# Performance work log

Hardware: AMD Instinct MI355X
Metric: run time of the kernel (lower is better)

## Reference

```python
import jax, jax.numpy as jnp
import numpy as np

HEADS = 12
DIM_HEAD = 64
WINDOW = 16
SHIFT = 1  # fixed stand-in for random.randint(0, window-1)
SCALE = DIM_HEAD ** -0.5


def window_cls_mask(n, window, shift):
    # Shifted block-diagonal mask over the n-1 non-CLS tokens, CLS attends/attended everywhere.
    size = n - 1
    idx = jnp.arange(size)
    cur = (idx - shift) % window
    left = jnp.clip(idx - cur, 0, size)
    right = jnp.clip(idx + (window - cur), 0, size)
    i = idx[:, None]  # query position
    wmask = (i >= left[None, :]) & (i < right[None, :])  # [size, size]
    full = jnp.ones((n, n), dtype=bool)
    full = full.at[1:, 1:].set(wmask)
    return full  # [n, n] bool


def setup_inputs() -> dict:
    key = jax.random.key(0)
    k1, k2, k3 = jax.random.split(key, 3)
    b, n, dim = 2, 2049, 768
    inner = HEADS * DIM_HEAD
    return {
        "x": jax.random.normal(k1, (b, n, dim), dtype=jnp.float32),
        "w_qkv": jax.random.normal(k2, (dim, 3 * inner), dtype=jnp.float32) * 0.02,
        "w_out": jax.random.normal(k3, (inner, dim), dtype=jnp.float32) * 0.02,
        "b_out": jnp.zeros((dim,), dtype=jnp.float32),
    }


def reference(x, w_qkv, w_out, b_out):
    b, n, dim = x.shape
    h, d = HEADS, DIM_HEAD
    qkv = x @ w_qkv  # [b, n, 3*h*d]
    q, k, v = jnp.split(qkv, 3, axis=-1)
    # b n (h d) -> b h n d
    reshape = lambda t: t.reshape(b, n, h, d).transpose(0, 2, 1, 3)
    q, k, v = reshape(q), reshape(k), reshape(v)
    dots = jnp.einsum('bhid,bhjd->bhij', q, k) * SCALE  # [b, h, n, n]
    mask = window_cls_mask(n, WINDOW, SHIFT)  # [n, n]
    neg = -jnp.finfo(dots.dtype).max
    dots = jnp.where(mask[None, None], dots, neg)
    attn = jax.nn.softmax(dots, axis=-1)
    out = jnp.einsum('bhij,bhjd->bhid', attn, v)  # [b, h, n, d]
    out = out.transpose(0, 2, 1, 3).reshape(b, n, h * d)
    return out @ w_out + b_out
```

## Files before the change

kernel.cpp:

```cpp
#include <hip/hip_runtime.h>
#include <hip/hip_bf16.h>
#include <math.h>

typedef __attribute__((ext_vector_type(8))) __bf16 bf16x8;
typedef __attribute__((ext_vector_type(4))) float f32x4;

#define HEADS 12
#define DHEAD 64
#define NTOK 2049
#define BATCH 2
#define DIM 768
#define QKV3 2304
#define MROWS 4098
#define MP 4224
#define ATT_SCALE 0.125f
#define BKS 64
#define NSPLIT 33
#define PSTRIDE 68

#define CVT_BLOCKS 1584
#define TQKV_BX 72
#define TQKV_BLOCKS (72 * 24)
#define TOUT_BX 24
#define TOUT_BLOCKS (24 * 24)
#define PREP_BLOCKS (CVT_BLOCKS + TQKV_BLOCKS + TOUT_BLOCKS)
#define WIN_BLOCKS (BATCH * 129 * 3)

__global__ __launch_bounds__(256) void prep_kernel(const float* __restrict__ x,
                                                   const float* __restrict__ w_qkv,
                                                   const float* __restrict__ w_out,
                                                   __bf16* __restrict__ xb,
                                                   __bf16* __restrict__ wqkvT,
                                                   __bf16* __restrict__ woutT) {
  __shared__ float tile[32][33];
  const int b = blockIdx.x, tid = threadIdx.x;
  if (b < CVT_BLOCKS) {
    long e = ((long)b * 256 + tid) * 8;
    int row = (int)(e / DIM);
    bf16x8 v;
    if (row < MROWS) {
      const float4 a = *(const float4*)(x + e);
      const float4 c = *(const float4*)(x + e + 4);
      v[0] = (__bf16)a.x; v[1] = (__bf16)a.y; v[2] = (__bf16)a.z; v[3] = (__bf16)a.w;
      v[4] = (__bf16)c.x; v[5] = (__bf16)c.y; v[6] = (__bf16)c.z; v[7] = (__bf16)c.w;
    } else {
#pragma unroll
      for (int j = 0; j < 8; ++j) v[j] = (__bf16)0.f;
    }
    *(bf16x8*)(xb + e) = v;
    return;
  }
  const float* in;
  __bf16* outp;
  int C, bx, by;
  if (b < CVT_BLOCKS + TQKV_BLOCKS) {
    int idx = b - CVT_BLOCKS;
    bx = idx % TQKV_BX; by = idx / TQKV_BX;
    in = w_qkv; outp = wqkvT; C = QKV3;
  } else {
    int idx = b - CVT_BLOCKS - TQKV_BLOCKS;
    bx = idx % TOUT_BX; by = idx / TOUT_BX;
    in = w_out; outp = woutT; C = DIM;
  }
  const int R = DIM;
  const int c0 = bx * 32, r0 = by * 32;
  const int tx = tid & 31, ty = tid >> 5;
#pragma unroll
  for (int i = 0; i < 4; ++i) {
    int r = ty + i * 8;
    tile[r][tx] = in[(size_t)(r0 + r) * C + c0 + tx];
  }
  __syncthreads();
#pragma unroll
  for (int i = 0; i < 4; ++i) {
    int r = ty + i * 8;
    outp[(size_t)(c0 + r) * R + r0 + tx] = (__bf16)tile[tx][r];
  }
}

__global__ __launch_bounds__(256) void gemm_qkv_kernel(const __bf16* __restrict__ A,
                                                       const __bf16* __restrict__ Bt,
                                                       __bf16* __restrict__ C) {
  __shared__ __bf16 sA[2][64 * BKS];
  __shared__ __bf16 sB[2][128 * BKS];
  const int tid = threadIdx.x;
  const int w = tid >> 6, lane = tid & 63;
  const int m0 = blockIdx.y * 64, n0 = blockIdx.x * 128;
  const int wr = w >> 1, wc = w & 1;
  const int K = DIM;
  f32x4 acc[2][4] = {};

  const int srow = (w << 3) + (lane >> 3);
  const int scolE = ((lane & 7) ^ (lane >> 3)) << 3;
  const __bf16* gA = A + (size_t)(m0 + srow) * K + scolE;
  const __bf16* gB = Bt + (size_t)(n0 + srow) * K + scolE;
  const int nk = K / BKS;

#define STAGE_Q(buf, kt)                                                                 \
  do {                                                                                   \
    _Pragma("unroll")                                                                    \
    for (int it = 0; it < 2; ++it) {                                                     \
      __builtin_amdgcn_global_load_lds(                                                  \
          (const __attribute__((address_space(1))) void*)(gA + (size_t)(it * 32) * K + (kt)), \
          (__attribute__((address_space(3))) void*)(&sA[buf][(it << 11) + (w << 9)]), 16, 0, 0); \
    }                                                                                    \
    _Pragma("unroll")                                                                    \
    for (int it = 0; it < 4; ++it) {                                                     \
      __builtin_amdgcn_global_load_lds(                                                  \
          (const __attribute__((address_space(1))) void*)(gB + (size_t)(it * 32) * K + (kt)), \
          (__attribute__((address_space(3))) void*)(&sB[buf][(it << 11) + (w << 9)]), 16, 0, 0); \
    }                                                                                    \
  } while (0)

  STAGE_Q(0, 0);
  __syncthreads();

  const int sw0 = ((lane >> 4) ^ (lane & 7)) << 3;
  const int sw1 = sw0 ^ 32;
  const int rofA = (wr * 32 + (lane & 15)) * BKS;
  const int rofB = (wc * 64 + (lane & 15)) * BKS;

  for (int t = 0; t < nk; ++t) {
    const int cur = t & 1;
    if (t + 1 < nk) STAGE_Q(cur ^ 1, (t + 1) * BKS);
    const __bf16* bufA = sA[cur];
    const __bf16* bufB = sB[cur];
#pragma unroll
    for (int kk = 0; kk < BKS; kk += 32) {
      const int so = (kk == 0) ? sw0 : sw1;
      bf16x8 af[2], bfr[4];
#pragma unroll
      for (int m = 0; m < 2; ++m)
        af[m] = *(const bf16x8*)&bufA[rofA + m * 16 * BKS + so];
#pragma unroll
      for (int n = 0; n < 4; ++n)
        bfr[n] = *(const bf16x8*)&bufB[rofB + n * 16 * BKS + so];
#pragma unroll
      for (int m = 0; m < 2; ++m)
#pragma unroll
        for (int n = 0; n < 4; ++n)
          acc[m][n] = __builtin_amdgcn_mfma_f32_16x16x32_bf16(af[m], bfr[n], acc[m][n], 0, 0, 0);
    }
    __syncthreads();
  }
#undef STAGE_Q

#pragma unroll
  for (int m = 0; m < 2; ++m) {
#pragma unroll
    for (int n = 0; n < 4; ++n) {
      int col = n0 + wc * 64 + n * 16 + (lane & 15);
      int rbase = m0 + wr * 32 + m * 16 + ((lane >> 4) << 2);
#pragma unroll
      for (int r = 0; r < 4; ++r) {
        C[(size_t)(rbase + r) * QKV3 + col] = (__bf16)acc[m][n][r];
      }
    }
  }
}

__global__ __launch_bounds__(256) void gemm_out_kernel(const __bf16* __restrict__ A,
                                                       const __bf16* __restrict__ Bt,
                                                       float* __restrict__ Cv,
                                                       const float* __restrict__ bias) {
  __shared__ __bf16 sA[2][64 * BKS];
  __shared__ __bf16 sB[2][64 * BKS];
  const int tid = threadIdx.x;
  const int w = tid >> 6, lane = tid & 63;
  const int m0 = blockIdx.y * 64, n0 = blockIdx.x * 64;
  const int wr = w >> 1, wc = w & 1;
  const int K = DIM, N = DIM;
  f32x4 acc[2][2] = {};

  const int srow = (w << 3) + (lane >> 3);
  const int scol = ((lane & 7) ^ (lane >> 3)) << 3;
  const __bf16* gA = A + (size_t)(m0 + srow) * K + scol;
  const __bf16* gB = Bt + (size_t)(n0 + srow) * K + scol;
  const int nk = K / BKS;

#define STAGE_O(buf, kt)                                                                 \
  do {                                                                                   \
    _Pragma("unroll")                                                                    \
    for (int it = 0; it < 2; ++it) {                                                     \
      __builtin_amdgcn_global_load_lds(                                                  \
          (const __attribute__((address_space(1))) void*)(gA + (size_t)(it * 32) * K + (kt)), \
          (__attribute__((address_space(3))) void*)(&sA[buf][(it << 11) + (w << 9)]), 16, 0, 0); \
      __builtin_amdgcn_global_load_lds(                                                  \
          (const __attribute__((address_space(1))) void*)(gB + (size_t)(it * 32) * K + (kt)), \
          (__attribute__((address_space(3))) void*)(&sB[buf][(it << 11) + (w << 9)]), 16, 0, 0); \
    }                                                                                    \
  } while (0)

  STAGE_O(0, 0);
  __syncthreads();

  const int sw0 = ((lane >> 4) ^ (lane & 7)) << 3;
  const int sw1 = sw0 ^ 32;
  const int rofA = (wr * 32 + (lane & 15)) * BKS;
  const int rofB = (wc * 32 + (lane & 15)) * BKS;

  for (int t = 0; t < nk; ++t) {
    const int cur = t & 1;
    if (t + 1 < nk) STAGE_O(cur ^ 1, (t + 1) * BKS);
    const __bf16* bufA = sA[cur];
    const __bf16* bufB = sB[cur];
#pragma unroll
    for (int kk = 0; kk < BKS; kk += 32) {
      const int so = (kk == 0) ? sw0 : sw1;
      bf16x8 af[2], bfr[2];
#pragma unroll
      for (int m = 0; m < 2; ++m)
        af[m] = *(const bf16x8*)&bufA[rofA + m * 16 * BKS + so];
#pragma unroll
      for (int n = 0; n < 2; ++n)
        bfr[n] = *(const bf16x8*)&bufB[rofB + n * 16 * BKS + so];
#pragma unroll
      for (int m = 0; m < 2; ++m)
#pragma unroll
        for (int n = 0; n < 2; ++n)
          acc[m][n] = __builtin_amdgcn_mfma_f32_16x16x32_bf16(af[m], bfr[n], acc[m][n], 0, 0, 0);
    }
    __syncthreads();
  }
#undef STAGE_O

#pragma unroll
  for (int m = 0; m < 2; ++m) {
#pragma unroll
    for (int n = 0; n < 2; ++n) {
      int col = n0 + wc * 32 + n * 16 + (lane & 15);
      int rbase = m0 + wr * 32 + m * 16 + ((lane >> 4) << 2);
#pragma unroll
      for (int r = 0; r < 4; ++r) {
        int row = rbase + r;
        if (row < MROWS) Cv[(size_t)row * N + col] = acc[m][n][r] + bias[col];
      }
    }
  }
}

__global__ __launch_bounds__(64) void attn_fused_kernel(const __bf16* __restrict__ qkv,
                                                        __bf16* __restrict__ attnb,
                                                        float* __restrict__ part) {
  __shared__ float sp_lds[64];
  const int lane = threadIdx.x;

  if (blockIdx.x < WIN_BLOCKS) {
    int bidx = blockIdx.x;
    int hg = bidx % 3; bidx /= 3;
    int blk = bidx % 129;
    int bb = bidx / 129;
    int h = hg * 4 + (lane >> 4);
    int qi = lane & 15;
    int t0 = (blk == 0) ? 1 : 2 + 16 * (blk - 1);
    int nt = (blk == 0) ? 1 : ((NTOK - t0) < 16 ? (NTOK - t0) : 16);
    bool active = qi < nt;
    int qt = t0 + (active ? qi : nt - 1);
    const size_t base = (size_t)bb * NTOK * QKV3;

    float q[64];
    {
      const __bf16* qp = qkv + base + (size_t)qt * QKV3 + h * DHEAD;
#pragma unroll
      for (int d0 = 0; d0 < 64; d0 += 8) {
        bf16x8 v = *(const bf16x8*)(qp + d0);
#pragma unroll
        for (int j = 0; j < 8; ++j) q[d0 + j] = (float)v[j];
      }
    }

    float s[17];
    float mx = -3.4e38f;
#pragma unroll
    for (int j = 0; j < 17; ++j) {
      int jc = (j - 1) < (nt - 1) ? (j - 1) : (nt - 1);
      int kt = (j == 0) ? 0 : t0 + jc;
      const __bf16* kp = qkv + base + (size_t)kt * QKV3 + DIM + h * DHEAD;
      float dot = 0.f;
#pragma unroll
      for (int d0 = 0; d0 < 64; d0 += 8) {
        bf16x8 v = *(const bf16x8*)(kp + d0);
#pragma unroll
        for (int jj = 0; jj < 8; ++jj) dot = fmaf(q[d0 + jj], (float)v[jj], dot);
      }
      s[j] = (j <= nt) ? dot * ATT_SCALE : -3.4e38f;
      mx = fmaxf(mx, s[j]);
    }
    float sum = 0.f;
#pragma unroll
    for (int j = 0; j < 17; ++j) {
      s[j] = expf(s[j] - mx);
      sum += s[j];
    }
    float inv = 1.f / sum;

    float o[64];
#pragma unroll
    for (int d = 0; d < 64; ++d) o[d] = 0.f;
#pragma unroll
    for (int j = 0; j < 17; ++j) {
      int jc = (j - 1) < (nt - 1) ? (j - 1) : (nt - 1);
      int vt = (j == 0) ? 0 : t0 + jc;
      const __bf16* vp = qkv + base + (size_t)vt * QKV3 + 2 * DIM + h * DHEAD;
      float p = s[j];
#pragma unroll
      for (int d0 = 0; d0 < 64; d0 += 8) {
        bf16x8 v = *(const bf16x8*)(vp + d0);
#pragma unroll
        for (int jj = 0; jj < 8; ++jj) o[d0 + jj] = fmaf(p, (float)v[jj], o[d0 + jj]);
      }
    }

    if (active) {
      __bf16* op = attnb + (size_t)(bb * NTOK + qt) * DIM + h * DHEAD;
#pragma unroll
      for (int d0 = 0; d0 < 64; d0 += 8) {
        bf16x8 v;
#pragma unroll
        for (int j = 0; j < 8; ++j) v[j] = (__bf16)(o[d0 + j] * inv);
        *(bf16x8*)(op + d0) = v;
      }
    }
    return;
  }

  int bid = blockIdx.x - WIN_BLOCKS;
  const int sp = bid % NSPLIT;
  const int bh = bid / NSPLIT;
  const int h = bh % HEADS;
  const int bb = bh / HEADS;
  const size_t base = (size_t)bb * NTOK * QKV3;

  float q[64];
  {
    const __bf16* qp = qkv + base + h * DHEAD;
#pragma unroll
    for (int d0 = 0; d0 < 64; d0 += 8) {
      bf16x8 v = *(const bf16x8*)(qp + d0);
#pragma unroll
      for (int j = 0; j < 8; ++j) q[d0 + j] = (float)v[j];
    }
  }

  const int t = sp * 64 + lane;
  const bool valid = t < NTOK;
  const int tc = valid ? t : NTOK - 1;
  float dot = 0.f;
  {
    const __bf16* kp = qkv + base + (size_t)tc * QKV3 + DIM + h * DHEAD;
#pragma unroll
    for (int d0 = 0; d0 < 64; d0 += 8) {
      bf16x8 v = *(const bf16x8*)(kp + d0);
#pragma unroll
      for (int j = 0; j < 8; ++j) dot = fmaf(q[d0 + j], (float)v[j], dot);
    }
  }
  float s = valid ? dot * ATT_SCALE : -3.4e38f;

  float m = s;
#pragma unroll
  for (int off = 32; off > 0; off >>= 1) m = fmaxf(m, __shfl_xor(m, off, 64));
  float p = valid ? expf(s - m) : 0.f;
  float l = p;
#pragma unroll
  for (int off = 32; off > 0; off >>= 1) l += __shfl_xor(l, off, 64);

  sp_lds[lane] = p;
  __syncthreads();

  const int nt = (NTOK - sp * 64) < 64 ? (NTOK - sp * 64) : 64;
  float o = 0.f;
  const __bf16* vcol = qkv + base + (size_t)(sp * 64) * QKV3 + 2 * DIM + h * DHEAD + lane;
  for (int tt = 0; tt < nt; ++tt) {
    o = fmaf(sp_lds[tt], (float)vcol[(size_t)tt * QKV3], o);
  }

  float* pb = part + ((size_t)bh * NSPLIT + sp) * PSTRIDE;
  pb[lane] = o;
  if (lane == 0) { pb[64] = m; pb[65] = l; }
}

__global__ __launch_bounds__(64) void attn_cls_reduce(const float* __restrict__ part,
                                                      __bf16* __restrict__ attnb) {
  const int bh = blockIdx.x;
  const int h = bh % HEADS;
  const int bb = bh / HEADS;
  const int lane = threadIdx.x;
  const float* pb0 = part + (size_t)bh * NSPLIT * PSTRIDE;
  float M = -3.4e38f;
#pragma unroll
  for (int i = 0; i < NSPLIT; ++i) M = fmaxf(M, pb0[i * PSTRIDE + 64]);
  float L = 0.f, o = 0.f;
#pragma unroll
  for (int i = 0; i < NSPLIT; ++i) {
    float w = expf(pb0[i * PSTRIDE + 64] - M);
    L = fmaf(pb0[i * PSTRIDE + 65], w, L);
    o = fmaf(pb0[i * PSTRIDE + lane], w, o);
  }
  attnb[(size_t)(bb * NTOK) * DIM + h * DHEAD + lane] = (__bf16)(o / L);
}

extern "C" void kernel_launch(void* const* d_in, const int* in_sizes, int n_in,
                              void* d_out, int out_size, void* d_ws, size_t ws_size,
                              hipStream_t stream) {
  const float* x = (const float*)d_in[0];
  const float* w_qkv = (const float*)d_in[1];
  const float* w_out = (const float*)d_in[2];
  const float* b_out = (const float*)d_in[3];
  float* out = (float*)d_out;

  char* ws = (char*)d_ws;
  __bf16* xb    = (__bf16*)(ws);
  __bf16* wqkvT = (__bf16*)(ws + 6488064);
  __bf16* woutT = (__bf16*)(ws + 6488064 + 3538944);
  __bf16* qkvb  = (__bf16*)(ws + 6488064 + 3538944 + 1179648);
  __bf16* attnb = (__bf16*)(ws + 6488064 + 3538944 + 1179648 + 19464192);
  float*  clsp  = (float*)(ws + 6488064 + 3538944 + 1179648 + 19464192 + 6488064);

  prep_kernel<<<PREP_BLOCKS, 256, 0, stream>>>(x, w_qkv, w_out, xb, wqkvT, woutT);

  gemm_qkv_kernel<<<dim3(QKV3 / 128, MP / 64), 256, 0, stream>>>(xb, wqkvT, qkvb);

  attn_fused_kernel<<<WIN_BLOCKS + BATCH * HEADS * NSPLIT, 64, 0, stream>>>(qkvb, attnb, clsp);
  attn_cls_reduce<<<BATCH * HEADS, 64, 0, stream>>>(clsp, attnb);

  gemm_out_kernel<<<dim3(DIM / 64, MP / 64), 256, 0, stream>>>(attnb, woutT, out, b_out);
}
```

Baseline: 148.6 us.

## Add XCD-aware block swizzle to GEMMs and attention, use online softmax in window path

Flattens the GEMM and attention grids to 1D and remaps block ids so consecutive logical tiles land on the same XCD, improving L2 reuse of shared A/B rows and qkv data across the eight chiplets. Separately rewrites the windowed attention path as a single-pass online softmax with lazy rescaling (threshold 8), fusing the K and V loops and dropping the 17-entry score array. This cuts one pass of V loads and register pressure, at the cost of a data-dependent rescale branch.

```diff
diff --git a/kernel.cpp b/kernel.cpp
--- a/kernel.cpp
+++ b/kernel.cpp
@@ -25,6 +25,13 @@
 #define TOUT_BLOCKS (24 * 24)
 #define PREP_BLOCKS (CVT_BLOCKS + TQKV_BLOCKS + TOUT_BLOCKS)
 #define WIN_BLOCKS (BATCH * 129 * 3)
+#define ATTN_BLOCKS (WIN_BLOCKS + BATCH * HEADS * NSPLIT)
+
+__device__ __forceinline__ int xcd_swz(int o, int nwg) {
+  const int q = nwg >> 3, r = nwg & 7;
+  const int xcd = o & 7, i = o >> 3;
+  return (xcd < r ? xcd * (q + 1) : r * (q + 1) + (xcd - r) * q) + i;
+}
 
 __global__ __launch_bounds__(256) void prep_kernel(const float* __restrict__ x,
                                                    const float* __restrict__ w_qkv,
@@ -83,9 +90,11 @@
                                                        __bf16* __restrict__ C) {
   __shared__ __bf16 sA[2][64 * BKS];
   __shared__ __bf16 sB[2][128 * BKS];
+  const int wg = xcd_swz(blockIdx.x, (MP / 64) * (QKV3 / 128));
+  const int by = wg / (QKV3 / 128), bx = wg % (QKV3 / 128);
   const int tid = threadIdx.x;
   const int w = tid >> 6, lane = tid & 63;
-  const int m0 = blockIdx.y * 64, n0 = blockIdx.x * 128;
+  const int m0 = by * 64, n0 = bx * 128;
   const int wr = w >> 1, wc = w & 1;
   const int K = DIM;
   f32x4 acc[2][4] = {};
@@ -165,9 +174,11 @@
                                                        const float* __restrict__ bias) {
   __shared__ __bf16 sA[2][64 * BKS];
   __shared__ __bf16 sB[2][64 * BKS];
+  const int wg = xcd_swz(blockIdx.x, (MP / 64) * (DIM / 64));
+  const int by = wg / (DIM / 64), bx = wg % (DIM / 64);
   const int tid = threadIdx.x;
   const int w = tid >> 6, lane = tid & 63;
-  const int m0 = blockIdx.y * 64, n0 = blockIdx.x * 64;
+  const int m0 = by * 64, n0 = bx * 64;
   const int wr = w >> 1, wc = w & 1;
   const int K = DIM, N = DIM;
   f32x4 acc[2][2] = {};
@@ -244,9 +255,10 @@
                                                         float* __restrict__ part) {
   __shared__ float sp_lds[64];
   const int lane = threadIdx.x;
-
-  if (blockIdx.x < WIN_BLOCKS) {
-    int bidx = blockIdx.x;
+  const int wgid = xcd_swz(blockIdx.x, ATTN_BLOCKS);
+
+  if (wgid < WIN_BLOCKS) {
+    int bidx = wgid;
     int hg = bidx % 3; bidx /= 3;
     int blk = bidx % 129;
     int bb = bidx / 129;
@@ -269,13 +281,33 @@
       }
     }
 
-    float s[17];
-    float mx = -3.4e38f;
-#pragma unroll
-    for (int j = 0; j < 17; ++j) {
+    float o[64];
+    float m, l;
+    {
+      const __bf16* kp = qkv + base + DIM + h * DHEAD;
+      float dot = 0.f;
+#pragma unroll
+      for (int d0 = 0; d0 < 64; d0 += 8) {
+        bf16x8 v = *(const bf16x8*)(kp + d0);
+#pragma unroll
+        for (int jj = 0; jj < 8; ++jj) dot = fmaf(q[d0 + jj], (float)v[jj], dot);
+      }
+      m = dot * ATT_SCALE;
+      l = 1.f;
+      const __bf16* vp = qkv + base + 2 * DIM + h * DHEAD;
+#pragma unroll
+      for (int d0 = 0; d0 < 64; d0 += 8) {
+        bf16x8 v = *(const bf16x8*)(vp + d0);
+#pragma unroll
+        for (int jj = 0; jj < 8; ++jj) o[d0 + jj] = (float)v[jj];
+      }
+    }
+#pragma unroll
+    for (int j = 1; j < 17; ++j) {
       int jc = (j - 1) < (nt - 1) ? (j - 1) : (nt - 1);
-      int kt = (j == 0) ? 0 : t0 + jc;
+      int kt = t0 + jc;
       const __bf16* kp = qkv + base + (size_t)kt * QKV3 + DIM + h * DHEAD;
+      const __bf16* vp = kp + DIM;
       float dot = 0.f;
 #pragma unroll
       for (int d0 = 0; d0 < 64; d0 += 8) {
@@ -283,26 +315,16 @@
 #pragma unroll
         for (int jj = 0; jj < 8; ++jj) dot = fmaf(q[d0 + jj], (float)v[jj], dot);
       }
-      s[j] = (j <= nt) ? dot * ATT_SCALE : -3.4e38f;
-      mx = fmaxf(mx, s[j]);
-    }
-    float sum = 0.f;
-#pragma unroll
-    for (int j = 0; j < 17; ++j) {
-      s[j] = expf(s[j] - mx);
-      sum += s[j];
-    }
-    float inv = 1.f / sum;
-
-    float o[64];
-#pragma unroll
-    for (int d = 0; d < 64; ++d) o[d] = 0.f;
-#pragma unroll
-    for (int j = 0; j < 17; ++j) {
-      int jc = (j - 1) < (nt - 1) ? (j - 1) : (nt - 1);
-      int vt = (j == 0) ? 0 : t0 + jc;
-      const __bf16* vp = qkv + base + (size_t)vt * QKV3 + 2 * DIM + h * DHEAD;
-      float p = s[j];
+      float s = (j <= nt) ? dot * ATT_SCALE : -3.4e38f;
+      if (s > m + 8.f) {
+        float c = expf(m - s);
+        l *= c;
+#pragma unroll
+        for (int d = 0; d < 64; ++d) o[d] *= c;
+        m = s;
+      }
+      float p = expf(s - m);
+      l += p;
 #pragma unroll
       for (int d0 = 0; d0 < 64; d0 += 8) {
         bf16x8 v = *(const bf16x8*)(vp + d0);
@@ -312,6 +334,7 @@
     }
 
     if (active) {
+      float inv = 1.f / l;
       __bf16* op = attnb + (size_t)(bb * NTOK + qt) * DIM + h * DHEAD;
 #pragma unroll
       for (int d0 = 0; d0 < 64; d0 += 8) {
@@ -324,7 +347,7 @@
     return;
   }
 
-  int bid = blockIdx.x - WIN_BLOCKS;
+  int bid = wgid - WIN_BLOCKS;
   const int sp = bid % NSPLIT;
   const int bh = bid / NSPLIT;
   const int h = bh % HEADS;
@@ -419,10 +442,10 @@
 
   prep_kernel<<<PREP_BLOCKS, 256, 0, stream>>>(x, w_qkv, w_out, xb, wqkvT, woutT);
 
-  gemm_qkv_kernel<<<dim3(QKV3 / 128, MP / 64), 256, 0, stream>>>(xb, wqkvT, qkvb);
-
-  attn_fused_kernel<<<WIN_BLOCKS + BATCH * HEADS * NSPLIT, 64, 0, stream>>>(qkvb, attnb, clsp);
+  gemm_qkv_kernel<<<(MP / 64) * (QKV3 / 128), 256, 0, stream>>>(xb, wqkvT, qkvb);
+
+  attn_fused_kernel<<<ATTN_BLOCKS, 64, 0, stream>>>(qkvb, attnb, clsp);
   attn_cls_reduce<<<BATCH * HEADS, 64, 0, stream>>>(clsp, attnb);
 
-  gemm_out_kernel<<<dim3(DIM / 64, MP / 64), 256, 0, stream>>>(attnb, woutT, out, b_out);
-}
+  gemm_out_kernel<<<(MP / 64) * (DIM / 64), 256, 0, stream>>>(attnb, woutT, out, b_out);
+}
```

New measurement: 174.1 us. +17.2%, slower.
